# Optimization experiments

Measured on AMD Instinct MI355X. Metric: run time of the kernel, lower is better.

Reference implementation:

```python
import jax, jax.numpy as jnp
import numpy as np

N_NODES = 100000
K = 50000  # ceil(ratio * N) with ratio = nodes_out / nodes_in = 0.5


def setup_inputs() -> dict:
    key = jax.random.key(0)
    k1, k2, k3 = jax.random.split(key, 3)
    x = jax.random.normal(k1, (N_NODES, 256), dtype=jnp.float32)
    edge_index = jax.random.randint(k2, (2, 3200000), 0, N_NODES, dtype=jnp.int64)
    weight = jax.random.normal(k3, (256,), dtype=jnp.float32)
    return {"x": x, "edge_index": edge_index, "weight": weight}


def reference(x, edge_index, weight):
    # --- PyG TopKPooling forward ---
    # score_i = tanh( <x_i, w> / ||w|| )
    score = jnp.tanh((x @ weight) / jnp.linalg.norm(weight))  # [N]
    # select top-k nodes by score
    top_scores, perm = jax.lax.top_k(score, K)  # [K], [K]
    # gather features and gate by score (multiplier)
    x_out = x[perm] * top_scores[:, None]  # [K, C]
    # --- filter_adj: keep edges whose endpoints both survive, remap ids ---
    mapping = jnp.full((x.shape[0],), -1, dtype=edge_index.dtype)
    mapping = mapping.at[perm].set(jnp.arange(K, dtype=edge_index.dtype))
    new_edges = mapping[edge_index]  # [2, E], -1 where endpoint dropped
    valid = (new_edges[0] >= 0) & (new_edges[1] >= 0)
    # fixed-shape output: invalid edges marked -1 (torch returns a compacted
    # variable-length tensor; we keep E fixed for jit-compatibility)
    edge_out = jnp.where(valid[None, :], new_edges, -1)
    return x_out, edge_out
```

## Files before the change

### kernel.cpp

```cpp
#include <hip/hip_runtime.h>
#include <math.h>

#define N_NODES 100000
#define N_FEAT  256
#define K_SEL   50000
#define N_EDGES 3200000
#define NBUCKET 65536
#define NCHUNK  256

#define GATHER_BLOCKS (K_SEL / 4)
#define EDGE_BLOCKS   (N_EDGES / (4 * 256))

typedef float __attribute__((ext_vector_type(4))) floatx4;
typedef int   __attribute__((ext_vector_type(4))) intx4;

__device__ __forceinline__ unsigned long long descKey(double z) {
    unsigned long long u = (unsigned long long)__double_as_longlong(z);
    unsigned long long a = (u >> 63) ? ~u : (u | 0x8000000000000000ULL);
    return ~a;
}

__device__ __forceinline__ unsigned int bucketOfFloat(float zf) {
    unsigned int u = __float_as_uint(zf);
    unsigned int a = (u >> 31) ? ~u : (u | 0x80000000u);
    return (~a) >> 16;
}

__global__ void init_kernel(const float* __restrict__ w, double* __restrict__ norm,
                            int* __restrict__ hist, int* __restrict__ counter) {
    __shared__ double sd[256];
    int t = blockIdx.x * blockDim.x + threadIdx.x;
    hist[t] = 0;
    if (t == 0) counter[0] = 0;
    if (blockIdx.x == 0) {
        int tt = threadIdx.x;
        double v = (double)w[tt];
        sd[tt] = v * v;
        __syncthreads();
        for (int off = 128; off > 0; off >>= 1) {
            if (tt < off) sd[tt] += sd[tt + off];
            __syncthreads();
        }
        if (tt == 0) norm[0] = sqrt(sd[0]);
    }
}

__global__ void score_kernel(const float* __restrict__ x, const float* __restrict__ w,
                             unsigned long long* __restrict__ key64,
                             float* __restrict__ dotf, int* __restrict__ hist) {
    int row  = (int)((blockIdx.x * blockDim.x + threadIdx.x) >> 6);
    int lane = threadIdx.x & 63;
    if (row >= N_NODES) return;
    const float4 xv = ((const float4*)(x + (size_t)row * N_FEAT))[lane];
    const float4 wv = ((const float4*)w)[lane];
    double acc = (double)xv.x * (double)wv.x + (double)xv.y * (double)wv.y +
                 (double)xv.z * (double)wv.z + (double)xv.w * (double)wv.w;
    for (int m = 32; m >= 1; m >>= 1) acc += __shfl_xor(acc, m, 64);
    if (lane == 0) {
        key64[row] = descKey(acc);
        float df = (float)acc;
        dotf[row] = df;
        atomicAdd(&hist[bucketOfFloat(df)], 1);
    }
}

__global__ void __launch_bounds__(256) scan_kernel(const int* __restrict__ hist,
                                                   int* __restrict__ start,
                                                   int* __restrict__ chunkSums,
                                                   int* __restrict__ chunkOff,
                                                   int* __restrict__ counter) {
    __shared__ int s[256];
    __shared__ int lastFlag;
    int c = blockIdx.x, t = threadIdx.x;
    int v = hist[c * 256 + t];
    s[t] = v;
    __syncthreads();
    for (int off = 1; off < 256; off <<= 1) {
        int add = (t >= off) ? s[t - off] : 0;
        __syncthreads();
        s[t] += add;
        __syncthreads();
    }
    start[c * 256 + t] = s[t] - v;
    if (t == 0) {
        atomicExch(&chunkSums[c], s[255]);
        __threadfence();
        int old = atomicAdd(counter, 1);
        lastFlag = (old == NCHUNK - 1);
    }
    __syncthreads();
    if (!lastFlag) return;
    int w = atomicAdd(&chunkSums[t], 0);
    __syncthreads();
    s[t] = w;
    __syncthreads();
    for (int off = 1; off < 256; off <<= 1) {
        int add = (t >= off) ? s[t - off] : 0;
        __syncthreads();
        s[t] += add;
        __syncthreads();
    }
    chunkOff[t] = s[t] - w;
}

__global__ void scatter_kernel(const unsigned long long* __restrict__ key64,
                               const float* __restrict__ dotf,
                               int* __restrict__ start,
                               const int* __restrict__ chunkOff,
                               unsigned long long* __restrict__ slotKey,
                               int* __restrict__ slotIdx) {
    int i = blockIdx.x * blockDim.x + threadIdx.x;
    if (i >= N_NODES) return;
    int b = (int)bucketOfFloat(dotf[i]);
    int pos = atomicAdd(&start[b], 1) + chunkOff[b >> 8];
    slotKey[pos] = key64[i];
    slotIdx[pos] = i;
}

__global__ void rank_kernel(const unsigned long long* __restrict__ slotKey,
                            const int* __restrict__ slotIdx,
                            const int* __restrict__ start, const int* __restrict__ hist,
                            const int* __restrict__ chunkOff,
                            const float* __restrict__ dotf,
                            int* __restrict__ mapping, int* __restrict__ perm,
                            float* __restrict__ selDot) {
    int s = blockIdx.x * blockDim.x + threadIdx.x;
    if (s >= N_NODES) return;
    int i = slotIdx[s];
    float df = dotf[i];
    int b = (int)bucketOfFloat(df);
    int end = start[b] + chunkOff[b >> 8];
    int cnt = hist[b];
    int st = end - cnt;
    if (st >= K_SEL) {
        mapping[i] = -1;
        return;
    }
    int rank = 0;
    if (cnt > 1) {
        unsigned long long myKey = slotKey[s];
        for (int t = st; t < end; ++t) {
            unsigned long long k = slotKey[t];
            if (k < myKey || (k == myKey && slotIdx[t] < i)) ++rank;
        }
    }
    int p = st + rank;
    if (p < K_SEL) {
        mapping[i] = p;
        perm[p] = i;
        selDot[p] = df;
    } else {
        mapping[i] = -1;
    }
}

__global__ void out_kernel(const float* __restrict__ x, const int* __restrict__ perm,
                           const float* __restrict__ selDot,
                           const double* __restrict__ normp,
                           const int* __restrict__ ei, const int* __restrict__ mapping,
                           float* __restrict__ out) {
    if (blockIdx.x < GATHER_BLOCKS) {
        int tid = blockIdx.x * 256 + threadIdx.x;
        int r = tid >> 6;
        int c = (tid & 63) << 2;
        int src = perm[r];
        float sc = tanhf(selDot[r] / (float)normp[0]);
        float4 v = *(const float4*)(x + (size_t)src * N_FEAT + c);
        floatx4 o;
        o.x = v.x * sc; o.y = v.y * sc; o.z = v.z * sc; o.w = v.w * sc;
        __builtin_nontemporal_store(o, (floatx4*)(out + (size_t)r * N_FEAT + c));
    } else {
        int tid = (blockIdx.x - GATHER_BLOCKS) * 256 + threadIdx.x;
        int e = tid << 2;
        intx4 a = __builtin_nontemporal_load((const intx4*)(ei + e));
        intx4 b = __builtin_nontemporal_load((const intx4*)(ei + N_EDGES + e));
        float* oeu = out + (size_t)K_SEL * N_FEAT;
        float* oev = oeu + N_EDGES;
        int m0 = mapping[a.x], m1 = mapping[a.y], m2 = mapping[a.z], m3 = mapping[a.w];
        int n0 = mapping[b.x], n1 = mapping[b.y], n2 = mapping[b.z], n3 = mapping[b.w];
        floatx4 ou, ov;
        bool v0 = (m0 >= 0) && (n0 >= 0);
        bool v1 = (m1 >= 0) && (n1 >= 0);
        bool v2 = (m2 >= 0) && (n2 >= 0);
        bool v3 = (m3 >= 0) && (n3 >= 0);
        ou.x = v0 ? (float)m0 : -1.0f; ov.x = v0 ? (float)n0 : -1.0f;
        ou.y = v1 ? (float)m1 : -1.0f; ov.y = v1 ? (float)n1 : -1.0f;
        ou.z = v2 ? (float)m2 : -1.0f; ov.z = v2 ? (float)n2 : -1.0f;
        ou.w = v3 ? (float)m3 : -1.0f; ov.w = v3 ? (float)n3 : -1.0f;
        __builtin_nontemporal_store(ou, (floatx4*)(oeu + e));
        __builtin_nontemporal_store(ov, (floatx4*)(oev + e));
    }
}

extern "C" void kernel_launch(void* const* d_in, const int* in_sizes, int n_in,
                              void* d_out, int out_size, void* d_ws, size_t ws_size,
                              hipStream_t stream) {
    const float* x  = (const float*)d_in[0];
    const int*   ei = (const int*)d_in[1];
    const float* w  = (const float*)d_in[2];
    float* out = (float*)d_out;

    char* p = (char*)d_ws;
    double* d_norm = (double*)p;                          p += 16;
    unsigned long long* key64   = (unsigned long long*)p; p += (size_t)N_NODES * 8;
    unsigned long long* slotKey = (unsigned long long*)p; p += (size_t)N_NODES * 8;
    float* dotf    = (float*)p; p += (size_t)N_NODES * 4;
    int*   mapping = (int*)p;   p += (size_t)N_NODES * 4;
    int*   slotIdx = (int*)p;   p += (size_t)N_NODES * 4;
    int*   perm    = (int*)p;   p += (size_t)K_SEL * 4;
    float* selDot  = (float*)p; p += (size_t)K_SEL * 4;
    int*   hist    = (int*)p;   p += (size_t)NBUCKET * 4;
    int*   start   = (int*)p;   p += (size_t)NBUCKET * 4;
    int*   chunkSums = (int*)p; p += (size_t)NCHUNK * 4;
    int*   chunkOff  = (int*)p; p += (size_t)NCHUNK * 4;
    int*   counter   = (int*)p; p += 16;

    init_kernel<<<NBUCKET / 256, 256, 0, stream>>>(w, d_norm, hist, counter);

    int waves_blocks = (N_NODES * 64 + 255) / 256;
    score_kernel<<<waves_blocks, 256, 0, stream>>>(x, w, key64, dotf, hist);

    scan_kernel<<<NCHUNK, 256, 0, stream>>>(hist, start, chunkSums, chunkOff, counter);

    int node_blocks = (N_NODES + 255) / 256;
    scatter_kernel<<<node_blocks, 256, 0, stream>>>(key64, dotf, start, chunkOff,
                                                    slotKey, slotIdx);

    rank_kernel<<<node_blocks, 256, 0, stream>>>(slotKey, slotIdx, start, hist,
                                                 chunkOff, dotf, mapping, perm, selDot);

    out_kernel<<<GATHER_BLOCKS + EDGE_BLOCKS, 256, 0, stream>>>(x, perm, selDot, d_norm,
                                                                ei, mapping, out);
}
```

Baseline: 307.3 us.

## Restructure score pass, drop dotf buffer, store float mapping, fuse init into scan

The score kernel now uses 16 lanes per row with four float4 loads each, so one wave handles four rows instead of one and the shuffle reduction is shorter. The dotf array is removed: scatter and rank recover the float score by inverting the 64-bit sort key. The mapping is stored as float so the edge pass no longer converts int to float. The init kernel is replaced by a memset, and the weight-norm reduction moves into the scan kernel. Together these cut one launch plus some memory traffic and conversion work, at the cost of extra key decode arithmetic.

```diff
diff --git a/kernel.cpp b/kernel.cpp
--- a/kernel.cpp
+++ b/kernel.cpp
@@ -20,58 +20,65 @@
     return ~a;
 }
 
+__device__ __forceinline__ double invKey(unsigned long long k) {
+    unsigned long long a = ~k;
+    unsigned long long u = (a >> 63) ? (a & 0x7FFFFFFFFFFFFFFFULL) : ~a;
+    return __longlong_as_double((long long)u);
+}
+
 __device__ __forceinline__ unsigned int bucketOfFloat(float zf) {
     unsigned int u = __float_as_uint(zf);
     unsigned int a = (u >> 31) ? ~u : (u | 0x80000000u);
     return (~a) >> 16;
 }
 
-__global__ void init_kernel(const float* __restrict__ w, double* __restrict__ norm,
-                            int* __restrict__ hist, int* __restrict__ counter) {
-    __shared__ double sd[256];
-    int t = blockIdx.x * blockDim.x + threadIdx.x;
-    hist[t] = 0;
-    if (t == 0) counter[0] = 0;
-    if (blockIdx.x == 0) {
-        int tt = threadIdx.x;
-        double v = (double)w[tt];
-        sd[tt] = v * v;
-        __syncthreads();
-        for (int off = 128; off > 0; off >>= 1) {
-            if (tt < off) sd[tt] += sd[tt + off];
-            __syncthreads();
-        }
-        if (tt == 0) norm[0] = sqrt(sd[0]);
-    }
-}
-
-__global__ void score_kernel(const float* __restrict__ x, const float* __restrict__ w,
-                             unsigned long long* __restrict__ key64,
-                             float* __restrict__ dotf, int* __restrict__ hist) {
-    int row  = (int)((blockIdx.x * blockDim.x + threadIdx.x) >> 6);
-    int lane = threadIdx.x & 63;
-    if (row >= N_NODES) return;
-    const float4 xv = ((const float4*)(x + (size_t)row * N_FEAT))[lane];
-    const float4 wv = ((const float4*)w)[lane];
-    double acc = (double)xv.x * (double)wv.x + (double)xv.y * (double)wv.y +
-                 (double)xv.z * (double)wv.z + (double)xv.w * (double)wv.w;
-    for (int m = 32; m >= 1; m >>= 1) acc += __shfl_xor(acc, m, 64);
-    if (lane == 0) {
+__global__ void __launch_bounds__(256) score_kernel(
+        const float* __restrict__ x, const float* __restrict__ w,
+        unsigned long long* __restrict__ key64, int* __restrict__ hist) {
+    const int t    = threadIdx.x;
+    const int i    = t & 15;
+    const int g    = (t & 63) >> 4;
+    const int wid  = (blockIdx.x << 2) + (t >> 6);
+    const int row  = (wid << 2) + g;
+    const float4* xr = (const float4*)(x + (size_t)row * N_FEAT);
+    const float4* wr = (const float4*)w;
+    double acc = 0.0;
+#pragma unroll
+    for (int j = 0; j < 4; ++j) {
+        float4 xv = xr[i + 16 * j];
+        float4 wv = wr[i + 16 * j];
+        acc += (double)xv.x * (double)wv.x + (double)xv.y * (double)wv.y +
+               (double)xv.z * (double)wv.z + (double)xv.w * (double)wv.w;
+    }
+#pragma unroll
+    for (int m = 8; m >= 1; m >>= 1) acc += __shfl_xor(acc, m, 16);
+    if (i == 0) {
         key64[row] = descKey(acc);
-        float df = (float)acc;
-        dotf[row] = df;
-        atomicAdd(&hist[bucketOfFloat(df)], 1);
+        atomicAdd(&hist[bucketOfFloat((float)acc)], 1);
     }
 }
 
 __global__ void __launch_bounds__(256) scan_kernel(const int* __restrict__ hist,
+                                                   const float* __restrict__ w,
+                                                   double* __restrict__ normp,
                                                    int* __restrict__ start,
                                                    int* __restrict__ chunkSums,
                                                    int* __restrict__ chunkOff,
                                                    int* __restrict__ counter) {
     __shared__ int s[256];
+    __shared__ double sd[256];
     __shared__ int lastFlag;
     int c = blockIdx.x, t = threadIdx.x;
+    if (c == 0) {
+        double v = (double)w[t];
+        sd[t] = v * v;
+        __syncthreads();
+        for (int off = 128; off > 0; off >>= 1) {
+            if (t < off) sd[t] += sd[t + off];
+            __syncthreads();
+        }
+        if (t == 0) normp[0] = sqrt(sd[0]);
+    }
     int v = hist[c * 256 + t];
     s[t] = v;
     __syncthreads();
@@ -90,9 +97,9 @@
     }
     __syncthreads();
     if (!lastFlag) return;
-    int w = atomicAdd(&chunkSums[t], 0);
-    __syncthreads();
-    s[t] = w;
+    int wsum = atomicAdd(&chunkSums[t], 0);
+    __syncthreads();
+    s[t] = wsum;
     __syncthreads();
     for (int off = 1; off < 256; off <<= 1) {
         int add = (t >= off) ? s[t - off] : 0;
@@ -100,20 +107,20 @@
         s[t] += add;
         __syncthreads();
     }
-    chunkOff[t] = s[t] - w;
+    chunkOff[t] = s[t] - wsum;
 }
 
 __global__ void scatter_kernel(const unsigned long long* __restrict__ key64,
-                               const float* __restrict__ dotf,
                                int* __restrict__ start,
                                const int* __restrict__ chunkOff,
                                unsigned long long* __restrict__ slotKey,
                                int* __restrict__ slotIdx) {
     int i = blockIdx.x * blockDim.x + threadIdx.x;
     if (i >= N_NODES) return;
-    int b = (int)bucketOfFloat(dotf[i]);
+    unsigned long long k = key64[i];
+    int b = (int)bucketOfFloat((float)invKey(k));
     int pos = atomicAdd(&start[b], 1) + chunkOff[b >> 8];
-    slotKey[pos] = key64[i];
+    slotKey[pos] = k;
     slotIdx[pos] = i;
 }
 
@@ -121,43 +128,43 @@
                             const int* __restrict__ slotIdx,
                             const int* __restrict__ start, const int* __restrict__ hist,
                             const int* __restrict__ chunkOff,
-                            const float* __restrict__ dotf,
-                            int* __restrict__ mapping, int* __restrict__ perm,
+                            float* __restrict__ mappingF, int* __restrict__ perm,
                             float* __restrict__ selDot) {
     int s = blockIdx.x * blockDim.x + threadIdx.x;
     if (s >= N_NODES) return;
+    unsigned long long myKey = slotKey[s];
     int i = slotIdx[s];
-    float df = dotf[i];
+    float df = (float)invKey(myKey);
     int b = (int)bucketOfFloat(df);
     int end = start[b] + chunkOff[b >> 8];
     int cnt = hist[b];
     int st = end - cnt;
     if (st >= K_SEL) {
-        mapping[i] = -1;
+        mappingF[i] = -1.0f;
         return;
     }
     int rank = 0;
     if (cnt > 1) {
-        unsigned long long myKey = slotKey[s];
-        for (int t = st; t < end; ++t) {
-            unsigned long long k = slotKey[t];
-            if (k < myKey || (k == myKey && slotIdx[t] < i)) ++rank;
+        for (int q = st; q < end; ++q) {
+            unsigned long long k = slotKey[q];
+            if (k < myKey || (k == myKey && slotIdx[q] < i)) ++rank;
         }
     }
     int p = st + rank;
     if (p < K_SEL) {
-        mapping[i] = p;
+        mappingF[i] = (float)p;
         perm[p] = i;
         selDot[p] = df;
     } else {
-        mapping[i] = -1;
+        mappingF[i] = -1.0f;
     }
 }
 
 __global__ void out_kernel(const float* __restrict__ x, const int* __restrict__ perm,
                            const float* __restrict__ selDot,
                            const double* __restrict__ normp,
-                           const int* __restrict__ ei, const int* __restrict__ mapping,
+                           const int* __restrict__ ei,
+                           const float* __restrict__ mappingF,
                            float* __restrict__ out) {
     if (blockIdx.x < GATHER_BLOCKS) {
         int tid = blockIdx.x * 256 + threadIdx.x;
@@ -176,17 +183,19 @@
         intx4 b = __builtin_nontemporal_load((const intx4*)(ei + N_EDGES + e));
         float* oeu = out + (size_t)K_SEL * N_FEAT;
         float* oev = oeu + N_EDGES;
-        int m0 = mapping[a.x], m1 = mapping[a.y], m2 = mapping[a.z], m3 = mapping[a.w];
-        int n0 = mapping[b.x], n1 = mapping[b.y], n2 = mapping[b.z], n3 = mapping[b.w];
+        float m0 = mappingF[a.x], m1 = mappingF[a.y];
+        float m2 = mappingF[a.z], m3 = mappingF[a.w];
+        float n0 = mappingF[b.x], n1 = mappingF[b.y];
+        float n2 = mappingF[b.z], n3 = mappingF[b.w];
         floatx4 ou, ov;
-        bool v0 = (m0 >= 0) && (n0 >= 0);
-        bool v1 = (m1 >= 0) && (n1 >= 0);
-        bool v2 = (m2 >= 0) && (n2 >= 0);
-        bool v3 = (m3 >= 0) && (n3 >= 0);
-        ou.x = v0 ? (float)m0 : -1.0f; ov.x = v0 ? (float)n0 : -1.0f;
-        ou.y = v1 ? (float)m1 : -1.0f; ov.y = v1 ? (float)n1 : -1.0f;
-        ou.z = v2 ? (float)m2 : -1.0f; ov.z = v2 ? (float)n2 : -1.0f;
-        ou.w = v3 ? (float)m3 : -1.0f; ov.w = v3 ? (float)n3 : -1.0f;
+        bool v0 = (m0 >= 0.0f) && (n0 >= 0.0f);
+        bool v1 = (m1 >= 0.0f) && (n1 >= 0.0f);
+        bool v2 = (m2 >= 0.0f) && (n2 >= 0.0f);
+        bool v3 = (m3 >= 0.0f) && (n3 >= 0.0f);
+        ou.x = v0 ? m0 : -1.0f; ov.x = v0 ? n0 : -1.0f;
+        ou.y = v1 ? m1 : -1.0f; ov.y = v1 ? n1 : -1.0f;
+        ou.z = v2 ? m2 : -1.0f; ov.z = v2 ? n2 : -1.0f;
+        ou.w = v3 ? m3 : -1.0f; ov.w = v3 ? n3 : -1.0f;
         __builtin_nontemporal_store(ou, (floatx4*)(oeu + e));
         __builtin_nontemporal_store(ov, (floatx4*)(oev + e));
     }
@@ -204,31 +213,30 @@
     double* d_norm = (double*)p;                          p += 16;
     unsigned long long* key64   = (unsigned long long*)p; p += (size_t)N_NODES * 8;
     unsigned long long* slotKey = (unsigned long long*)p; p += (size_t)N_NODES * 8;
-    float* dotf    = (float*)p; p += (size_t)N_NODES * 4;
-    int*   mapping = (int*)p;   p += (size_t)N_NODES * 4;
-    int*   slotIdx = (int*)p;   p += (size_t)N_NODES * 4;
-    int*   perm    = (int*)p;   p += (size_t)K_SEL * 4;
-    float* selDot  = (float*)p; p += (size_t)K_SEL * 4;
-    int*   hist    = (int*)p;   p += (size_t)NBUCKET * 4;
-    int*   start   = (int*)p;   p += (size_t)NBUCKET * 4;
-    int*   chunkSums = (int*)p; p += (size_t)NCHUNK * 4;
-    int*   chunkOff  = (int*)p; p += (size_t)NCHUNK * 4;
-    int*   counter   = (int*)p; p += 16;
-
-    init_kernel<<<NBUCKET / 256, 256, 0, stream>>>(w, d_norm, hist, counter);
-
-    int waves_blocks = (N_NODES * 64 + 255) / 256;
-    score_kernel<<<waves_blocks, 256, 0, stream>>>(x, w, key64, dotf, hist);
-
-    scan_kernel<<<NCHUNK, 256, 0, stream>>>(hist, start, chunkSums, chunkOff, counter);
+    float* mappingF = (float*)p; p += (size_t)N_NODES * 4;
+    int*   slotIdx  = (int*)p;   p += (size_t)N_NODES * 4;
+    int*   perm     = (int*)p;   p += (size_t)K_SEL * 4;
+    float* selDot   = (float*)p; p += (size_t)K_SEL * 4;
+    int*   hist     = (int*)p;   p += (size_t)NBUCKET * 4;
+    int*   counter  = (int*)p;   p += 16;
+    int*   start    = (int*)p;   p += (size_t)NBUCKET * 4;
+    int*   chunkSums= (int*)p;   p += (size_t)NCHUNK * 4;
+    int*   chunkOff = (int*)p;   p += (size_t)NCHUNK * 4;
+
+    hipMemsetAsync(hist, 0, (size_t)NBUCKET * 4 + 16, stream);
+
+    score_kernel<<<N_NODES / 16, 256, 0, stream>>>(x, w, key64, hist);
+
+    scan_kernel<<<NCHUNK, 256, 0, stream>>>(hist, w, d_norm, start, chunkSums,
+                                            chunkOff, counter);
 
     int node_blocks = (N_NODES + 255) / 256;
-    scatter_kernel<<<node_blocks, 256, 0, stream>>>(key64, dotf, start, chunkOff,
+    scatter_kernel<<<node_blocks, 256, 0, stream>>>(key64, start, chunkOff,
                                                     slotKey, slotIdx);
 
     rank_kernel<<<node_blocks, 256, 0, stream>>>(slotKey, slotIdx, start, hist,
-                                                 chunkOff, dotf, mapping, perm, selDot);
+                                                 chunkOff, mappingF, perm, selDot);
 
     out_kernel<<<GATHER_BLOCKS + EDGE_BLOCKS, 256, 0, stream>>>(x, perm, selDot, d_norm,
-                                                                ei, mapping, out);
-}
+                                                                ei, mappingF, out);
+}
```

New measurement: 337.7 us. 1.1x slower.
